# Kernel optimization log

Hardware: AMD Instinct MI355X
Metric: run time of the kernel (lower is better)

## Reference

```python
import jax, jax.numpy as jnp
import numpy as np

SPATIAL_SHAPES = np.array([[128, 128], [64, 64], [32, 32], [16, 16]], dtype=np.int32)  # (H, W) per level
D_MODEL = 256
D_FFN = 1024
N_LEVELS = 4
N_HEADS = 8
N_POINTS = 4
HEAD_DIM = D_MODEL // N_HEADS
B = 2
LEN = int((SPATIAL_SHAPES[:, 0] * SPATIAL_SHAPES[:, 1]).sum())  # 21760


def layer_norm(x, g, b, eps=1e-5):
    mu = x.mean(-1, keepdims=True)
    var = ((x - mu) ** 2).mean(-1, keepdims=True)
    return (x - mu) / jnp.sqrt(var + eps) * g + b


def ms_deform_attn_core(value, sampling_locations, attention_weights):
    # value: [B, Len, M, D]; locations: [B, Lq, M, L, P, 2] in [0,1]; weights: [B, Lq, M, L, P]
    B_, _, M, D = value.shape
    Lq = sampling_locations.shape[1]
    P = sampling_locations.shape[4]
    out = jnp.zeros((B_, M, Lq, D), value.dtype)
    start = 0
    for lvl, (H, W) in enumerate(SPATIAL_SHAPES.tolist()):
        v = value[:, start:start + H * W].transpose(0, 2, 1, 3)  # [B, M, H*W, D]
        start += H * W
        loc = sampling_locations[:, :, :, lvl].transpose(0, 2, 1, 3, 4)  # [B, M, Lq, P, 2]
        # grid_sample semantics: align_corners=False, padding_mode='zeros'
        x = loc[..., 0] * W - 0.5
        y = loc[..., 1] * H - 0.5
        x0 = jnp.floor(x)
        y0 = jnp.floor(y)
        wx = (x - x0)[..., None]
        wy = (y - y0)[..., None]

        def gather(xi, yi):
            valid = ((xi >= 0) & (xi < W) & (yi >= 0) & (yi < H)).astype(value.dtype)
            idx = (jnp.clip(yi, 0, H - 1) * W + jnp.clip(xi, 0, W - 1)).astype(jnp.int32)
            idx = idx.reshape(B_, M, Lq * P)
            g = jnp.take_along_axis(v, idx[..., None], axis=2).reshape(B_, M, Lq, P, D)
            return g * valid[..., None]

        v00 = gather(x0, y0)
        v01 = gather(x0 + 1, y0)
        v10 = gather(x0, y0 + 1)
        v11 = gather(x0 + 1, y0 + 1)
        samp = (v00 * (1 - wx) + v01 * wx) * (1 - wy) + (v10 * (1 - wx) + v11 * wx) * wy
        w_l = attention_weights[:, :, :, lvl].transpose(0, 2, 1, 3)  # [B, M, Lq, P]
        out = out + (samp * w_l[..., None]).sum(axis=3)
    return out.transpose(0, 2, 1, 3).reshape(B_, Lq, M * D)


def setup_inputs() -> dict:
    key = jax.random.key(0)
    ks = jax.random.split(key, 16)
    f32 = jnp.float32

    def lin(k, fan_in, fan_out, scale=None):
        s = scale if scale is not None else 1.0 / np.sqrt(fan_in)
        return jax.random.normal(k, (fan_in, fan_out), f32) * s

    starts = np.concatenate([[0], np.cumsum(SPATIAL_SHAPES[:, 0] * SPATIAL_SHAPES[:, 1])[:-1]]).astype(np.int32)
    inp = {
        "src": jax.random.normal(ks[0], (B, LEN, D_MODEL), f32),
        "pos": jax.random.normal(ks[1], (B, LEN, D_MODEL), f32),
        "reference_points": jax.random.uniform(ks[2], (B, LEN, N_LEVELS, 2), f32),
        "spatial_shapes": jnp.asarray(SPATIAL_SHAPES),
        "level_start_index": jnp.asarray(starts),
        "norm1_g": jnp.ones((D_MODEL,), f32), "norm1_b": jnp.zeros((D_MODEL,), f32),
        "norm2_g": jnp.ones((D_MODEL,), f32), "norm2_b": jnp.zeros((D_MODEL,), f32),
        "W_value": lin(ks[3], D_MODEL, D_MODEL), "b_value": jnp.zeros((D_MODEL,), f32),
        "W_off": lin(ks[4], D_MODEL, N_HEADS * N_LEVELS * N_POINTS * 2, scale=0.01),
        "b_off": jax.random.normal(ks[5], (N_HEADS * N_LEVELS * N_POINTS * 2,), f32) * 0.01,
        "W_attn": lin(ks[6], D_MODEL, N_HEADS * N_LEVELS * N_POINTS),
        "b_attn": jnp.zeros((N_HEADS * N_LEVELS * N_POINTS,), f32),
        "W_out": lin(ks[7], D_MODEL, D_MODEL), "b_out": jnp.zeros((D_MODEL,), f32),
        "W_ffn1": lin(ks[8], D_MODEL, D_FFN), "b_ffn1": jnp.zeros((D_FFN,), f32),
        "W_ffn2": lin(ks[9], D_FFN, D_MODEL), "b_ffn2": jnp.zeros((D_MODEL,), f32),
    }
    return inp


def reference(src, pos, reference_points, spatial_shapes, level_start_index,
              norm1_g, norm1_b, norm2_g, norm2_b,
              W_value, b_value, W_off, b_off, W_attn, b_attn, W_out, b_out,
              W_ffn1, b_ffn1, W_ffn2, b_ffn2):
    B_, Lq, C = src.shape
    # pre-norm deformable self-attention; NOTE: value path uses un-normed src (faithful to source)
    q = layer_norm(src, norm1_g, norm1_b) + pos
    value = (src @ W_value + b_value).reshape(B_, Lq, N_HEADS, HEAD_DIM)
    offsets = (q @ W_off + b_off).reshape(B_, Lq, N_HEADS, N_LEVELS, N_POINTS, 2)
    attn = jax.nn.softmax((q @ W_attn + b_attn).reshape(B_, Lq, N_HEADS, N_LEVELS * N_POINTS), axis=-1)
    attn = attn.reshape(B_, Lq, N_HEADS, N_LEVELS, N_POINTS)
    offset_normalizer = spatial_shapes[..., ::-1].astype(src.dtype)  # (W, H) per level
    loc = reference_points[:, :, None, :, None, :] + offsets / offset_normalizer[None, None, None, :, None, :]
    attn_out = ms_deform_attn_core(value, loc, attn) @ W_out + b_out
    src = src + attn_out
    h = layer_norm(src, norm2_g, norm2_b)
    h = jax.nn.gelu(h @ W_ffn1 + b_ffn1, approximate=False) @ W_ffn2 + b_ffn2
    return src + h
```

## Files before the change

### kernel.cpp

```cpp
#include <hip/hip_runtime.h>
#include <hip/hip_bf16.h>
#include <math.h>

#define LEN_TOT 21760
#define BATCH 2
#define MROWS (BATCH * LEN_TOT)
#define DMODEL 256
#define DFFN 1024

typedef unsigned short ushort_t;
typedef __attribute__((ext_vector_type(8))) short short8;
typedef __attribute__((ext_vector_type(4))) float floatx4;

__device__ __forceinline__ ushort_t f2b(float f) {
    unsigned u = __float_as_uint(f);
    unsigned r = (u + 0x7FFFu + ((u >> 16) & 1u)) >> 16;
    return (ushort_t)r;
}

struct TP {
    const float* s[6];
    ushort_t*    d[6];
    int K[6];
    int N[6];
    int start[7];
};

__global__ __launch_bounds__(256) void transpose_convert(TP tp) {
    __shared__ float tile[32][33];
    int blk = blockIdx.x;
    int seg = 0;
    while (seg < 5 && blk >= tp.start[seg + 1]) seg++;
    int local = blk - tp.start[seg];
    int K = tp.K[seg], N = tp.N[seg];
    int tn = N >> 5;
    int k0 = (local / tn) << 5, n0 = (local % tn) << 5;
    int r = threadIdx.x >> 5, c = threadIdx.x & 31;
    const float* src = tp.s[seg];
    #pragma unroll
    for (int rr = r; rr < 32; rr += 8)
        tile[rr][c] = src[(size_t)(k0 + rr) * N + n0 + c];
    __syncthreads();
    ushort_t* dst = tp.d[seg];
    #pragma unroll
    for (int rr = r; rr < 32; rr += 8)
        dst[(size_t)(n0 + rr) * K + k0 + c] = f2b(tile[c][rr]);
}

__global__ __launch_bounds__(256) void ln_dual_kernel(
    const float* __restrict__ x, const float* __restrict__ g,
    const float* __restrict__ bb, const float* __restrict__ addv,
    ushort_t* __restrict__ y_bf, ushort_t* __restrict__ x_bf)
{
    int row  = blockIdx.x * 4 + (threadIdx.x >> 6);
    int lane = threadIdx.x & 63;
    size_t base = (size_t)row * DMODEL + lane * 4;
    float4 v = *(const float4*)(x + base);

    float s = v.x + v.y + v.z + v.w;
    #pragma unroll
    for (int o = 32; o; o >>= 1) s += __shfl_xor(s, o, 64);
    float mu = s * (1.0f / 256.0f);

    float d0 = v.x - mu, d1 = v.y - mu, d2 = v.z - mu, d3 = v.w - mu;
    float vs = d0*d0 + d1*d1 + d2*d2 + d3*d3;
    #pragma unroll
    for (int o = 32; o; o >>= 1) vs += __shfl_xor(vs, o, 64);
    float rstd = rsqrtf(vs * (1.0f / 256.0f) + 1e-5f);

    float4 gv = *(const float4*)(g  + lane * 4);
    float4 bv = *(const float4*)(bb + lane * 4);
    float o0 = d0 * rstd * gv.x + bv.x;
    float o1 = d1 * rstd * gv.y + bv.y;
    float o2 = d2 * rstd * gv.z + bv.z;
    float o3 = d3 * rstd * gv.w + bv.w;
    if (addv) {
        float4 av = *(const float4*)(addv + base);
        o0 += av.x; o1 += av.y; o2 += av.z; o3 += av.w;
    }
    ushort4 ob = {f2b(o0), f2b(o1), f2b(o2), f2b(o3)};
    *(ushort4*)(y_bf + base) = ob;
    if (x_bf) {
        ushort4 xb = {f2b(v.x), f2b(v.y), f2b(v.z), f2b(v.w)};
        *(ushort4*)(x_bf + base) = xb;
    }
}

template<int GELU_ACT, int HAS_RES, int OUT_BF16>
__global__ __launch_bounds__(256) void gemm_mfma(
    const ushort_t* __restrict__ A, const ushort_t* __restrict__ Bt,
    const float* __restrict__ bias, const float* __restrict__ res,
    float* __restrict__ C, ushort_t* __restrict__ Cbf,
    int M, int N, int K)
{
    constexpr int BM = 128, BK = 32;
    constexpr int LDA = BK + 8;
    __shared__ __align__(16) ushort_t As[BM * LDA];
    __shared__ __align__(16) ushort_t Bs[BM * LDA];

    const int tid  = threadIdx.x;
    const int wave = tid >> 6;
    const int lane = tid & 63;
    const int wm = (wave & 1) * 64;
    const int wn = (wave >> 1) * 64;
    const int ml = lane & 15;
    const int quad = lane >> 4;
    const int m0 = blockIdx.y * BM, n0 = blockIdx.x * BM;

    floatx4 acc[4][4] = {};

    for (int k0 = 0; k0 < K; k0 += BK) {
        #pragma unroll
        for (int it = 0; it < 2; it++) {
            int idx = tid + it * 256;
            int r = idx >> 2, seg = idx & 3;
            *(short8*)(As + r * LDA + seg * 8) =
                *(const short8*)(A + (size_t)(m0 + r) * K + k0 + seg * 8);
            *(short8*)(Bs + r * LDA + seg * 8) =
                *(const short8*)(Bt + (size_t)(n0 + r) * K + k0 + seg * 8);
        }
        __syncthreads();

        short8 af[4], bfr[4];
        #pragma unroll
        for (int i = 0; i < 4; i++)
            af[i] = *(const short8*)(As + (wm + i * 16 + ml) * LDA + quad * 8);
        #pragma unroll
        for (int j = 0; j < 4; j++)
            bfr[j] = *(const short8*)(Bs + (wn + j * 16 + ml) * LDA + quad * 8);
        #pragma unroll
        for (int i = 0; i < 4; i++)
            #pragma unroll
            for (int j = 0; j < 4; j++)
                acc[i][j] = __builtin_amdgcn_mfma_f32_16x16x32_bf16(
                    af[i], bfr[j], acc[i][j], 0, 0, 0);
        __syncthreads();
    }

    #pragma unroll
    for (int j = 0; j < 4; j++) {
        int col = n0 + wn + j * 16 + ml;
        float bc = bias[col];
        #pragma unroll
        for (int i = 0; i < 4; i++) {
            int row = m0 + wm + i * 16 + quad * 4;
            #pragma unroll
            for (int r = 0; r < 4; r++) {
                float v = acc[i][j][r] + bc;
                if (GELU_ACT) {
                    v = 0.5f * v * (1.0f + erff(v * 0.7071067811865476f));
                }
                if (HAS_RES) v += res[(size_t)(row + r) * N + col];
                if (OUT_BF16) Cbf[(size_t)(row + r) * N + col] = f2b(v);
                else          C[(size_t)(row + r) * N + col] = v;
            }
        }
    }
}

__global__ __launch_bounds__(256) void msdeform_kernel(
    const float* __restrict__ value, const float* __restrict__ offs,
    const float* __restrict__ logits, const float* __restrict__ refp,
    ushort_t* __restrict__ out_bf)
{
    int gid = blockIdx.x * 8 + (threadIdx.x >> 5);
    int l   = threadIdx.x & 31;
    int bq  = gid >> 3;
    int m   = gid & 7;
    int b   = (bq >= LEN_TOT) ? 1 : 0;

    int i = l & 15;
    float logit = logits[(size_t)gid * 16 + i];
    float mx = logit;
    #pragma unroll
    for (int o = 8; o; o >>= 1) mx = fmaxf(mx, __shfl_xor(mx, o, 32));
    float e = __expf(logit - mx);
    float se = e;
    #pragma unroll
    for (int o = 8; o; o >>= 1) se += __shfl_xor(se, o, 32);
    float prob = e / se;

    int lvl = i >> 2;
    int Wl  = 128 >> lvl;
    float Wf = (float)Wl;
    const int ST_[4] = {0, 16384, 20480, 21504};

    float2 off2 = ((const float2*)offs)[(size_t)gid * 16 + i];
    float2 ref2 = ((const float2*)refp)[(size_t)bq * 4 + lvl];
    float xs = fmaf(ref2.x, Wf, off2.x) - 0.5f;
    float ys = fmaf(ref2.y, Wf, off2.y) - 0.5f;
    float xf = floorf(xs), yf = floorf(ys);
    int x0 = (int)xf, y0 = (int)yf;
    float wx = xs - xf, wy = ys - yf;
    float wx1 = 1.0f - wx, wy1 = 1.0f - wy;

    bool vx0 = (x0 >= 0) & (x0 < Wl);
    bool vx1 = (x0 + 1 >= 0) & (x0 + 1 < Wl);
    bool vy0 = (y0 >= 0) & (y0 < Wl);
    bool vy1 = (y0 + 1 >= 0) & (y0 + 1 < Wl);
    int cx0 = min(max(x0, 0), Wl - 1);
    int cx1 = min(max(x0 + 1, 0), Wl - 1);
    int cy0 = min(max(y0, 0), Wl - 1);
    int cy1 = min(max(y0 + 1, 0), Wl - 1);

    int vbase = b * LEN_TOT + ST_[lvl];
    int i00 = (vbase + cy0 * Wl + cx0) * 256 + m * 32;
    int i01 = (vbase + cy0 * Wl + cx1) * 256 + m * 32;
    int i10 = (vbase + cy1 * Wl + cx0) * 256 + m * 32;
    int i11 = (vbase + cy1 * Wl + cx1) * 256 + m * 32;
    float w00 = (vx0 && vy0) ? prob * wx1 * wy1 : 0.0f;
    float w01 = (vx1 && vy0) ? prob * wx  * wy1 : 0.0f;
    float w10 = (vx0 && vy1) ? prob * wx1 * wy  : 0.0f;
    float w11 = (vx1 && vy1) ? prob * wx  * wy  : 0.0f;

    int sA = l >> 2;
    int cA = l & 3;
    int t0 = __shfl(i00, sA, 32), t1 = __shfl(i01, sA, 32);
    int t2 = __shfl(i10, sA, 32), t3 = __shfl(i11, sA, 32);
    int addrA = (cA == 0) ? t0 : (cA == 1) ? t1 : (cA == 2) ? t2 : t3;
    float u0 = __shfl(w00, sA, 32), u1 = __shfl(w01, sA, 32);
    float u2 = __shfl(w10, sA, 32), u3 = __shfl(w11, sA, 32);
    float wA = (cA == 0) ? u0 : (cA == 1) ? u1 : (cA == 2) ? u2 : u3;
    t0 = __shfl(i00, sA + 8, 32); t1 = __shfl(i01, sA + 8, 32);
    t2 = __shfl(i10, sA + 8, 32); t3 = __shfl(i11, sA + 8, 32);
    int addrB = (cA == 0) ? t0 : (cA == 1) ? t1 : (cA == 2) ? t2 : t3;
    u0 = __shfl(w00, sA + 8, 32); u1 = __shfl(w01, sA + 8, 32);
    u2 = __shfl(w10, sA + 8, 32); u3 = __shfl(w11, sA + 8, 32);
    float wB = (cA == 0) ? u0 : (cA == 1) ? u1 : (cA == 2) ? u2 : u3;

    int cl = l >> 3;
    int d4 = l & 7;
    float ax = 0.0f, ay = 0.0f, az = 0.0f, aw = 0.0f;
    #pragma unroll
    for (int s = 0; s < 8; s++) {
        int   a = __shfl(addrA, s * 4 + cl, 32);
        float w = __shfl(wA,    s * 4 + cl, 32);
        float4 v = *(const float4*)(value + a + (d4 << 2));
        ax = fmaf(w, v.x, ax); ay = fmaf(w, v.y, ay);
        az = fmaf(w, v.z, az); aw = fmaf(w, v.w, aw);
    }
    #pragma unroll
    for (int s = 0; s < 8; s++) {
        int   a = __shfl(addrB, s * 4 + cl, 32);
        float w = __shfl(wB,    s * 4 + cl, 32);
        float4 v = *(const float4*)(value + a + (d4 << 2));
        ax = fmaf(w, v.x, ax); ay = fmaf(w, v.y, ay);
        az = fmaf(w, v.z, az); aw = fmaf(w, v.w, aw);
    }
    ax += __shfl_xor(ax, 8, 32);  ay += __shfl_xor(ay, 8, 32);
    az += __shfl_xor(az, 8, 32);  aw += __shfl_xor(aw, 8, 32);
    ax += __shfl_xor(ax, 16, 32); ay += __shfl_xor(ay, 16, 32);
    az += __shfl_xor(az, 16, 32); aw += __shfl_xor(aw, 16, 32);

    if (l < 8) {
        ushort4 o = {f2b(ax), f2b(ay), f2b(az), f2b(aw)};
        *(ushort4*)(out_bf + (size_t)gid * 32 + (d4 << 2)) = o;
    }
}

extern "C" void kernel_launch(void* const* d_in, const int* in_sizes, int n_in,
                              void* d_out, int out_size, void* d_ws, size_t ws_size,
                              hipStream_t stream)
{
    const float* src  = (const float*)d_in[0];
    const float* pos  = (const float*)d_in[1];
    const float* refp = (const float*)d_in[2];
    const float* n1g = (const float*)d_in[5];
    const float* n1b = (const float*)d_in[6];
    const float* n2g = (const float*)d_in[7];
    const float* n2b = (const float*)d_in[8];
    const float* Wv  = (const float*)d_in[9];
    const float* bv  = (const float*)d_in[10];
    const float* Wof = (const float*)d_in[11];
    const float* bof = (const float*)d_in[12];
    const float* Wat = (const float*)d_in[13];
    const float* bat = (const float*)d_in[14];
    const float* Wo  = (const float*)d_in[15];
    const float* bo  = (const float*)d_in[16];
    const float* Wf1 = (const float*)d_in[17];
    const float* bf1 = (const float*)d_in[18];
    const float* Wf2 = (const float*)d_in[19];
    const float* bf2 = (const float*)d_in[20];
    float* out = (float*)d_out;

    char* ws = (char*)d_ws;
    const int M = MROWS;
    const size_t SZ_BF = (size_t)M * 256 * 2;
    const size_t SZ_F  = (size_t)M * 256 * 4;

    ushort_t* q_bf    = (ushort_t*)(ws);
    float*    value   = (float*)   (ws + SZ_BF);
    ushort_t* src_bf  = (ushort_t*)(ws + SZ_BF + SZ_F);
    float*    offsb   = (float*)   (ws + 2 * SZ_BF + SZ_F);
    float*    logitsb = (float*)   (ws + 2 * SZ_BF + 2 * SZ_F);
    ushort_t* h0_bf   = q_bf;
    ushort_t* sampled = src_bf;
    float*    src2    = value;
    ushort_t* h1_bf   = src_bf;
    char* wtp = ws + 2 * SZ_BF + 2 * SZ_F + (size_t)M * 128 * 4;
    ushort_t* WvT  = (ushort_t*)(wtp);
    ushort_t* WofT = WvT  + 256 * 256;
    ushort_t* WatT = WofT + 256 * 256;
    ushort_t* WoT  = WatT + 256 * 128;
    ushort_t* Wf1T = WoT  + 256 * 256;
    ushort_t* Wf2T = Wf1T + 256 * 1024;

    TP tp;
    tp.s[0] = Wv;  tp.d[0] = WvT;  tp.K[0] = 256;  tp.N[0] = 256;
    tp.s[1] = Wof; tp.d[1] = WofT; tp.K[1] = 256;  tp.N[1] = 256;
    tp.s[2] = Wat; tp.d[2] = WatT; tp.K[2] = 256;  tp.N[2] = 128;
    tp.s[3] = Wo;  tp.d[3] = WoT;  tp.K[3] = 256;  tp.N[3] = 256;
    tp.s[4] = Wf1; tp.d[4] = Wf1T; tp.K[4] = 256;  tp.N[4] = 1024;
    tp.s[5] = Wf2; tp.d[5] = Wf2T; tp.K[5] = 1024; tp.N[5] = 256;
    tp.start[0] = 0;   tp.start[1] = 64;  tp.start[2] = 128;
    tp.start[3] = 160; tp.start[4] = 224; tp.start[5] = 480; tp.start[6] = 736;
    transpose_convert<<<736, 256, 0, stream>>>(tp);

    ln_dual_kernel<<<M / 4, 256, 0, stream>>>(src, n1g, n1b, pos, q_bf, src_bf);
    gemm_mfma<0, 0, 0><<<dim3(2, M / 128), 256, 0, stream>>>(
        src_bf, WvT, bv, nullptr, value, nullptr, M, 256, 256);
    gemm_mfma<0, 0, 0><<<dim3(2, M / 128), 256, 0, stream>>>(
        q_bf, WofT, bof, nullptr, offsb, nullptr, M, 256, 256);
    gemm_mfma<0, 0, 0><<<dim3(1, M / 128), 256, 0, stream>>>(
        q_bf, WatT, bat, nullptr, logitsb, nullptr, M, 128, 256);
    msdeform_kernel<<<M, 256, 0, stream>>>(value, offsb, logitsb, refp, sampled);
    gemm_mfma<0, 1, 0><<<dim3(2, M / 128), 256, 0, stream>>>(
        sampled, WoT, bo, src, src2, nullptr, M, 256, 256);
    ln_dual_kernel<<<M / 4, 256, 0, stream>>>(src2, n2g, n2b, nullptr, h0_bf, nullptr);
    gemm_mfma<1, 0, 1><<<dim3(8, M / 128), 256, 0, stream>>>(
        h0_bf, Wf1T, bf1, nullptr, nullptr, h1_bf, M, 1024, 256);
    gemm_mfma<0, 1, 0><<<dim3(2, M / 128), 256, 0, stream>>>(
        h1_bf, Wf2T, bf2, src2, out, nullptr, M, 256, 1024);
}
```

Measured before the change: 517.0 us.

## Load GEMM tiles via global_load_lds and stage bf16 epilogue through LDS

The GEMM tile loads now use direct global-to-LDS DMA (global_load_lds), which skips the register round trip. The LDS padding is dropped so the layout matches the linear order the DMA writes. The bf16 output path writes each 16x64 sub-tile into LDS first, then stores it to global memory as coalesced 16-byte vectors instead of scattered 2-byte stores. Removing the padding may bring back LDS bank conflicts on the fragment reads. The epilogue relies only on lgkmcnt within a wave, with no barrier.

```diff
diff --git a/kernel.cpp b/kernel.cpp
--- a/kernel.cpp
+++ b/kernel.cpp
@@ -11,6 +11,8 @@
 typedef unsigned short ushort_t;
 typedef __attribute__((ext_vector_type(8))) short short8;
 typedef __attribute__((ext_vector_type(4))) float floatx4;
+typedef __attribute__((address_space(3))) ushort_t lds_us;
+typedef __attribute__((address_space(1))) const ushort_t glb_us;
 
 __device__ __forceinline__ ushort_t f2b(float f) {
     unsigned u = __float_as_uint(f);
@@ -94,9 +96,8 @@
     int M, int N, int K)
 {
     constexpr int BM = 128, BK = 32;
-    constexpr int LDA = BK + 8;
-    __shared__ __align__(16) ushort_t As[BM * LDA];
-    __shared__ __align__(16) ushort_t Bs[BM * LDA];
+    __shared__ __align__(16) ushort_t As[BM * BK];
+    __shared__ __align__(16) ushort_t Bs[BM * BK];
 
     const int tid  = threadIdx.x;
     const int wave = tid >> 6;
@@ -107,27 +108,29 @@
     const int quad = lane >> 4;
     const int m0 = blockIdx.y * BM, n0 = blockIdx.x * BM;
 
+    const int r0 = tid >> 2, s0 = tid & 3;
+    const int r1 = (tid + 256) >> 2;
+
     floatx4 acc[4][4] = {};
 
     for (int k0 = 0; k0 < K; k0 += BK) {
-        #pragma unroll
-        for (int it = 0; it < 2; it++) {
-            int idx = tid + it * 256;
-            int r = idx >> 2, seg = idx & 3;
-            *(short8*)(As + r * LDA + seg * 8) =
-                *(const short8*)(A + (size_t)(m0 + r) * K + k0 + seg * 8);
-            *(short8*)(Bs + r * LDA + seg * 8) =
-                *(const short8*)(Bt + (size_t)(n0 + r) * K + k0 + seg * 8);
-        }
+        const ushort_t* gA0 = A  + (size_t)(m0 + r0) * K + k0 + s0 * 8;
+        const ushort_t* gA1 = A  + (size_t)(m0 + r1) * K + k0 + s0 * 8;
+        const ushort_t* gB0 = Bt + (size_t)(n0 + r0) * K + k0 + s0 * 8;
+        const ushort_t* gB1 = Bt + (size_t)(n0 + r1) * K + k0 + s0 * 8;
+        __builtin_amdgcn_global_load_lds((glb_us*)gA0, (lds_us*)(As + tid * 8),        16, 0, 0);
+        __builtin_amdgcn_global_load_lds((glb_us*)gA1, (lds_us*)(As + (tid + 256) * 8),16, 0, 0);
+        __builtin_amdgcn_global_load_lds((glb_us*)gB0, (lds_us*)(Bs + tid * 8),        16, 0, 0);
+        __builtin_amdgcn_global_load_lds((glb_us*)gB1, (lds_us*)(Bs + (tid + 256) * 8),16, 0, 0);
         __syncthreads();
 
         short8 af[4], bfr[4];
         #pragma unroll
         for (int i = 0; i < 4; i++)
-            af[i] = *(const short8*)(As + (wm + i * 16 + ml) * LDA + quad * 8);
+            af[i] = *(const short8*)(As + (wm + i * 16 + ml) * BK + quad * 8);
         #pragma unroll
         for (int j = 0; j < 4; j++)
-            bfr[j] = *(const short8*)(Bs + (wn + j * 16 + ml) * LDA + quad * 8);
+            bfr[j] = *(const short8*)(Bs + (wn + j * 16 + ml) * BK + quad * 8);
         #pragma unroll
         for (int i = 0; i < 4; i++)
             #pragma unroll
@@ -137,22 +140,50 @@
         __syncthreads();
     }
 
-    #pragma unroll
-    for (int j = 0; j < 4; j++) {
-        int col = n0 + wn + j * 16 + ml;
-        float bc = bias[col];
+    if (OUT_BF16) {
+        ushort_t* pool  = (wave < 2) ? As : Bs;
+        ushort_t* wbase = pool + (wave & 1) * 2048;
+        const int lr  = lane >> 2;
+        const int sg  = lane & 3;
         #pragma unroll
         for (int i = 0; i < 4; i++) {
-            int row = m0 + wm + i * 16 + quad * 4;
+            ushort_t* wbuf = wbase + (i & 1) * 1024;
             #pragma unroll
-            for (int r = 0; r < 4; r++) {
-                float v = acc[i][j][r] + bc;
-                if (GELU_ACT) {
-                    v = 0.5f * v * (1.0f + erff(v * 0.7071067811865476f));
+            for (int j = 0; j < 4; j++) {
+                float bc = bias[n0 + wn + j * 16 + ml];
+                #pragma unroll
+                for (int r = 0; r < 4; r++) {
+                    float v = acc[i][j][r] + bc;
+                    if (GELU_ACT) v = 0.5f * v * (1.0f + erff(v * 0.7071067811865476f));
+                    if (HAS_RES)
+                        v += res[(size_t)(m0 + wm + i * 16 + quad * 4 + r) * N
+                                 + n0 + wn + j * 16 + ml];
+                    wbuf[(quad * 4 + r) * 64 + j * 16 + ml] = f2b(v);
                 }
-                if (HAS_RES) v += res[(size_t)(row + r) * N + col];
-                if (OUT_BF16) Cbf[(size_t)(row + r) * N + col] = f2b(v);
-                else          C[(size_t)(row + r) * N + col] = v;
+            }
+            asm volatile("s_waitcnt lgkmcnt(0)" ::: "memory");
+            #pragma unroll
+            for (int h = 0; h < 2; h++) {
+                short8 vv = *(const short8*)(wbuf + lr * 64 + (sg + 4 * h) * 8);
+                *(short8*)(Cbf + (size_t)(m0 + wm + i * 16 + lr) * N
+                                 + n0 + wn + (sg + 4 * h) * 8) = vv;
+            }
+        }
+    } else {
+        #pragma unroll
+        for (int j = 0; j < 4; j++) {
+            int col = n0 + wn + j * 16 + ml;
+            float bc = bias[col];
+            #pragma unroll
+            for (int i = 0; i < 4; i++) {
+                int row = m0 + wm + i * 16 + quad * 4;
+                #pragma unroll
+                for (int r = 0; r < 4; r++) {
+                    float v = acc[i][j][r] + bc;
+                    if (GELU_ACT) v = 0.5f * v * (1.0f + erff(v * 0.7071067811865476f));
+                    if (HAS_RES) v += res[(size_t)(row + r) * N + col];
+                    C[(size_t)(row + r) * N + col] = v;
+                }
             }
         }
     }
```

After: 505.1 us. 1.02x faster.
